# Optimization experiments

Hardware: AMD Instinct MI355X
Metric: run time of the kernel (lower is better)

The kernel has to match this reference:

```python
import jax, jax.numpy as jnp
import numpy as np

N_HEADS = 12


def setup_inputs() -> dict:
    key = jax.random.key(0)
    ks = jax.random.split(key, 3)
    B, N, C = 32, 1024, 768
    x = jax.random.normal(ks[0], (B, N, C), dtype=jnp.float32)
    w_qkv = jax.random.normal(ks[1], (C, 3 * C), dtype=jnp.float32) * (1.0 / np.sqrt(C))
    b_qkv = jnp.zeros((3 * C,), dtype=jnp.float32)
    w_out = jax.random.normal(ks[2], (C, C), dtype=jnp.float32) * (1.0 / np.sqrt(C))
    b_out = jnp.zeros((C,), dtype=jnp.float32)
    return {"x": x, "w_qkv": w_qkv, "b_qkv": b_qkv, "w_out": w_out, "b_out": b_out}


def reference(x, w_qkv, b_qkv, w_out, b_out):
    B, N, C = x.shape
    H = N_HEADS
    D = C // H  # head_dim
    qkv = (x @ w_qkv + b_qkv).reshape(B, N, 3, H, D)
    qkv = jnp.transpose(qkv, (2, 0, 3, 1, 4))
    q, k, v = qkv[0], qkv[1], qkv[2]
    # channel attention: k^T @ v -> (B,H,D,D), scaled by sqrt(head_dim)
    attn = jnp.einsum("bhnd,bhne->bhde", k, v) / np.sqrt(D).astype(np.float32)
    attn = jax.nn.softmax(attn, axis=-1)
    # attn @ q^T -> (B,H,D,N); swapaxes -> (B,H,N,D)
    out = jnp.einsum("bhde,bhne->bhnd", attn, q)
    # ProjOut: merge heads (B,N,C) + Dense(C)
    out = jnp.transpose(out, (0, 2, 1, 3)).reshape(B, N, C)
    return out @ w_out + b_out
```

## Files before the change

kernel.cpp:

```cpp
#include <hip/hip_runtime.h>
#include <hip/hip_bf16.h>
#include <stdint.h>
#include <stddef.h>

#define B_ 32
#define N_ 1024
#define C_ 768
#define H_ 12
#define D_ 64
#define M_ (B_*N_)
#define TC_ (3*C_)

typedef __bf16 bf16_t;
typedef __attribute__((ext_vector_type(8))) __bf16 bf16x8;
typedef __attribute__((ext_vector_type(4))) __bf16 bf16x4;
typedef __attribute__((ext_vector_type(4))) float  f32x4;

#define MFMA16(a,b,c) __builtin_amdgcn_mfma_f32_16x16x32_bf16(a,b,c,0,0,0)

__device__ __forceinline__ void lds_load16(const void* g, void* l) {
  __builtin_amdgcn_global_load_lds(
      (const __attribute__((address_space(1))) void*)g,
      (__attribute__((address_space(3))) void*)l, 16, 0, 0);
}

__global__ void cvt_bf16(const float* __restrict__ in, bf16_t* __restrict__ out, int n) {
  int i = (blockIdx.x * 256 + threadIdx.x) * 8;
  if (i >= n) return;
  const float4 a = *(const float4*)(in + i);
  const float4 b = *(const float4*)(in + i + 4);
  bf16x8 r;
  r[0]=(bf16_t)a.x; r[1]=(bf16_t)a.y; r[2]=(bf16_t)a.z; r[3]=(bf16_t)a.w;
  r[4]=(bf16_t)b.x; r[5]=(bf16_t)b.y; r[6]=(bf16_t)b.z; r[7]=(bf16_t)b.w;
  *(bf16x8*)(out + i) = r;
}

__global__ void transpose_cvt(const float* __restrict__ in, bf16_t* __restrict__ out,
                              int R, int Cc) {
  __shared__ float t[32][33];
  const int c0 = blockIdx.x * 32, r0 = blockIdx.y * 32;
  const int tx = threadIdx.x & 31, ty = threadIdx.x >> 5;
  #pragma unroll
  for (int k = 0; k < 4; ++k)
    t[ty + k*8][tx] = in[(size_t)(r0 + ty + k*8)*Cc + c0 + tx];
  __syncthreads();
  #pragma unroll
  for (int k = 0; k < 4; ++k)
    out[(size_t)(c0 + ty + k*8)*R + r0 + tx] = (bf16_t)t[tx][ty + k*8];
}

template<int MODE>
__global__ __launch_bounds__(256, 2)
void gemm_bt(const bf16_t* __restrict__ A, const bf16_t* __restrict__ BT,
             const float* __restrict__ bias, float* __restrict__ Cout,
             bf16_t* __restrict__ qh,
             bf16_t* __restrict__ kthi, bf16_t* __restrict__ vthi,
             int K, int Ndim, int nbx)
{
  __shared__ __align__(16) char smem[34816];
  bf16_t* As   = (bf16_t*)smem;
  bf16_t* Bs   = (bf16_t*)(smem + 8192);
  bf16_t* tile = (bf16_t*)smem;

  const int nwg = gridDim.x;
  const int cpx = nwg >> 3;
  const int bid = blockIdx.x;
  const int swz = (bid & 7) * cpx + (bid >> 3);
  const int bx  = swz % nbx;
  const int by  = swz / nbx;

  const int tid  = threadIdx.x;
  const int wave = tid >> 6;
  const int lane = tid & 63;
  const int rowBase = by * 128;
  const int colBase = bx * 128;
  const int wr = (wave >> 1) * 64;
  const int wc = (wave &  1) * 64;
  const int fr = lane & 15;
  const int fo = (lane >> 4) * 8;
  const int e  = tid * 8;
  const int r0t = e >> 5;
  const int c0t = e & 31;

  const bf16_t* Ap = A  + (size_t)(rowBase + r0t) * K + c0t;
  const bf16_t* Bp = BT + (size_t)(colBase + r0t) * K + c0t;

  f32x4 acc[4][4] = {{0.f,0.f,0.f,0.f}};

  for (int k0 = 0; k0 < K; k0 += 32) {
    lds_load16(Ap + k0,                 &As[wave*512]);
    lds_load16(Ap + (size_t)64*K + k0,  &As[2048 + wave*512]);
    lds_load16(Bp + k0,                 &Bs[wave*512]);
    lds_load16(Bp + (size_t)64*K + k0,  &Bs[2048 + wave*512]);
    __syncthreads();
    bf16x8 af[4], bfv[4];
    #pragma unroll
    for (int m = 0; m < 4; ++m) af[m]  = *(const bf16x8*)&As[(wr + m*16 + fr)*32 + fo];
    #pragma unroll
    for (int n = 0; n < 4; ++n) bfv[n] = *(const bf16x8*)&Bs[(wc + n*16 + fr)*32 + fo];
    #pragma unroll
    for (int m = 0; m < 4; ++m)
      #pragma unroll
      for (int n = 0; n < 4; ++n)
        acc[m][n] = MFMA16(af[m], bfv[n], acc[m][n]);
    __syncthreads();
  }

  if (MODE == 0) {
    #pragma unroll
    for (int n = 0; n < 4; ++n) {
      const int gc = colBase + wc + n*16 + fr;
      const float bb = bias[gc];
      #pragma unroll
      for (int m = 0; m < 4; ++m) {
        const int gr = rowBase + wr + m*16 + ((lane >> 4) << 2);
        #pragma unroll
        for (int j = 0; j < 4; ++j)
          Cout[(size_t)(gr + j)*Ndim + gc] = acc[m][n][j] + bb;
      }
    }
  } else {
    #pragma unroll
    for (int n = 0; n < 4; ++n) {
      const int c  = wc + n*16 + fr;
      const float bb = bias[colBase + c];
      #pragma unroll
      for (int m = 0; m < 4; ++m) {
        const int r0 = wr + m*16 + ((lane >> 4) << 2);
        bf16x4 hv;
        hv[0]=(bf16_t)(acc[m][n][0]+bb); hv[1]=(bf16_t)(acc[m][n][1]+bb);
        hv[2]=(bf16_t)(acc[m][n][2]+bb); hv[3]=(bf16_t)(acc[m][n][3]+bb);
        *(bf16x4*)&tile[c*136 + r0] = hv;
      }
    }
    __syncthreads();
    const int s   = colBase / C_;
    const int b   = rowBase >> 10;
    const int nn0 = rowBase & (N_ - 1);
    if (s == 0) {
      const int r  = tid >> 1, ch = tid & 1;
      const int h  = (colBase >> 6) + ch;
      bf16_t* dst = qh + (((size_t)b*H_ + h)*N_ + nn0 + r)*D_;
      #pragma unroll
      for (int i0 = 0; i0 < 64; i0 += 8) {
        bf16x8 vv;
        #pragma unroll
        for (int i = 0; i < 8; ++i) vv[i] = tile[(ch*64 + i0 + i)*136 + r];
        *(bf16x8*)&dst[i0] = vv;
      }
    } else {
      const int c  = tid >> 1, rh = tid & 1;
      const int rem = colBase + c - s*C_;
      const int h = rem >> 6, d = rem & 63;
      bf16_t* dst = (s == 1 ? kthi : vthi)
                    + (((size_t)b*H_ + h)*D_ + d)*N_ + nn0 + rh*64;
      #pragma unroll
      for (int i0 = 0; i0 < 64; i0 += 8)
        *(bf16x8*)&dst[i0] = *(const bf16x8*)&tile[c*136 + rh*64 + i0];
    }
  }
}

__global__ __launch_bounds__(256, 2)
void attn_softmax_k(const bf16_t* __restrict__ kthi, const bf16_t* __restrict__ vthi,
                    bf16_t* __restrict__ attn)
{
  __shared__ float tile[64][65];
  const int bh = blockIdx.x;
  const int tid = threadIdx.x, wave = tid >> 6, lane = tid & 63;
  const int fr = lane & 15, fo = (lane >> 4) * 8;
  const size_t base = (size_t)bh * D_ * N_;
  f32x4 acc[4][4] = {{0.f,0.f,0.f,0.f}};
  const int k0lo = wave * 256;
  #pragma unroll 1
  for (int k0 = k0lo; k0 < k0lo + 256; k0 += 32) {
    bf16x8 ah[4], bhv[4];
    #pragma unroll
    for (int m = 0; m < 4; ++m)
      ah[m] = *(const bf16x8*)&kthi[base + (size_t)(m*16 + fr)*N_ + k0 + fo];
    #pragma unroll
    for (int n = 0; n < 4; ++n)
      bhv[n] = *(const bf16x8*)&vthi[base + (size_t)(n*16 + fr)*N_ + k0 + fo];
    #pragma unroll
    for (int m = 0; m < 4; ++m)
      #pragma unroll
      for (int n = 0; n < 4; ++n)
        acc[m][n] = MFMA16(ah[m], bhv[n], acc[m][n]);
  }
  for (int w = 0; w < 4; ++w) {
    if (wave == w) {
      #pragma unroll
      for (int m = 0; m < 4; ++m)
        #pragma unroll
        for (int n = 0; n < 4; ++n) {
          const int row = m*16 + ((lane >> 4) << 2);
          const int col = n*16 + fr;
          #pragma unroll
          for (int j = 0; j < 4; ++j) {
            if (w == 0) tile[row+j][col]  = acc[m][n][j];
            else        tile[row+j][col] += acc[m][n][j];
          }
        }
    }
    __syncthreads();
  }
  if (tid < 64) {
    float mx = -3.0e38f;
    #pragma unroll
    for (int c = 0; c < 64; ++c) mx = fmaxf(mx, tile[tid][c]);
    mx *= 0.125f;
    float ssum = 0.f;
    #pragma unroll
    for (int c = 0; c < 64; ++c) {
      const float ev = __expf(tile[tid][c]*0.125f - mx);
      tile[tid][c] = ev;
      ssum += ev;
    }
    const float inv = 1.0f / ssum;
    bf16_t* ao = attn + (size_t)bh * D_ * D_ + tid * D_;
    #pragma unroll
    for (int c = 0; c < 64; ++c) ao[c] = (bf16_t)(tile[tid][c] * inv);
  }
}

__global__ __launch_bounds__(256, 2)
void attn_apply(const bf16_t* __restrict__ qh, const bf16_t* __restrict__ attn,
                bf16_t* __restrict__ y2)
{
  const int bh = blockIdx.y;
  const int b = bh / H_, h = bh - b*H_;
  const int tid = threadIdx.x, wave = tid >> 6, lane = tid & 63;
  const int fr = lane & 15, fo = (lane >> 4) * 8;
  const int n0 = blockIdx.x * 256 + wave * 64;
  const bf16_t* qb = qh   + (size_t)bh * N_ * D_;
  const bf16_t* ab = attn + (size_t)bh * D_ * D_;
  f32x4 acc[4][4] = {{0.f,0.f,0.f,0.f}};
  #pragma unroll
  for (int k0 = 0; k0 < 64; k0 += 32) {
    bf16x8 af[4], bfv[4];
    #pragma unroll
    for (int m = 0; m < 4; ++m)
      af[m] = *(const bf16x8*)&qb[(size_t)(n0 + m*16 + fr)*D_ + k0 + fo];
    #pragma unroll
    for (int n = 0; n < 4; ++n)
      bfv[n] = *(const bf16x8*)&ab[(n*16 + fr)*D_ + k0 + fo];
    #pragma unroll
    for (int m = 0; m < 4; ++m)
      #pragma unroll
      for (int n = 0; n < 4; ++n)
        acc[m][n] = MFMA16(af[m], bfv[n], acc[m][n]);
  }
  #pragma unroll
  for (int m = 0; m < 4; ++m) {
    const int nr = n0 + m*16 + ((lane >> 4) << 2);
    #pragma unroll
    for (int n = 0; n < 4; ++n) {
      const int d = n*16 + fr;
      #pragma unroll
      for (int j = 0; j < 4; ++j)
        y2[(size_t)(b*N_ + nr + j)*C_ + h*D_ + d] = (bf16_t)acc[m][n][j];
    }
  }
}

extern "C" void kernel_launch(void* const* d_in, const int* in_sizes, int n_in,
                              void* d_out, int out_size, void* d_ws, size_t ws_size,
                              hipStream_t stream)
{
  (void)in_sizes; (void)n_in; (void)out_size;
  const float* x     = (const float*)d_in[0];
  const float* w_qkv = (const float*)d_in[1];
  const float* b_qkv = (const float*)d_in[2];
  const float* w_out = (const float*)d_in[3];
  const float* b_out = (const float*)d_in[4];
  float* out = (float*)d_out;

  const size_t sz_xb   = (size_t)M_*C_*2;
  const size_t sz_wq   = (size_t)TC_*C_*2;
  const size_t sz_wo   = (size_t)C_*C_*2;
  const size_t sz_qh   = (size_t)B_*H_*N_*D_*2;
  const size_t sz_kv   = (size_t)B_*H_*D_*N_*2;
  const size_t sz_attn = (size_t)B_*H_*D_*D_*2;

  char* p = (char*)d_ws;
  bf16_t* xb    = (bf16_t*)p; p += sz_xb;
  bf16_t* wqkvT = (bf16_t*)p; p += sz_wq;
  bf16_t* woutT = (bf16_t*)p; p += sz_wo;
  bf16_t* qh    = (bf16_t*)p; p += sz_qh;
  bf16_t* kthi  = (bf16_t*)p; p += sz_kv;
  bf16_t* vthi  = (bf16_t*)p; p += sz_kv;
  bf16_t* attn  = (bf16_t*)p; p += sz_attn;
  const size_t base_need = (size_t)(p - (char*)d_ws);
  bf16_t* y2 = xb;

  if (ws_size < base_need) return;

  cvt_bf16<<<dim3((M_*C_)/2048), 256, 0, stream>>>(x, xb, M_*C_);
  transpose_cvt<<<dim3(TC_/32, C_/32), 256, 0, stream>>>(w_qkv, wqkvT, C_, TC_);
  transpose_cvt<<<dim3(C_/32,  C_/32), 256, 0, stream>>>(w_out, woutT, C_, C_);

  gemm_bt<1><<<dim3((TC_/128)*(M_/128)), 256, 0, stream>>>(
      xb, wqkvT, b_qkv, nullptr, qh, kthi, vthi, C_, 0, TC_/128);

  attn_softmax_k<<<dim3(B_*H_), 256, 0, stream>>>(kthi, vthi, attn);

  attn_apply<<<dim3(N_/256, B_*H_), 256, 0, stream>>>(qh, attn, y2);

  gemm_bt<0><<<dim3((C_/128)*(M_/128)), 256, 0, stream>>>(
      y2, woutT, b_out, out, nullptr, nullptr, nullptr, C_, C_, C_/128);
}
```

Measured before the change: 300.9 us.

## Fold attention into per-batch output weights and switch GEMM to 32x32 MFMA

Removes the attn_apply pass and its y2 intermediate by composing each batch's attention matrices with the output projection weights into a per-batch weight matrix. The final GEMM then reads q directly in head-major layout. The GEMM core moves from 16x16x32 to 32x32x16 MFMA and adds an XOR swizzle on the LDS layout to reduce bank conflicts. This trades a large activation round trip for a small per-batch weight composition, at the cost of an extra bf16 rounding of the composed weights.

```diff
diff --git a/kernel.cpp b/kernel.cpp
--- a/kernel.cpp
+++ b/kernel.cpp
@@ -15,8 +15,10 @@
 typedef __attribute__((ext_vector_type(8))) __bf16 bf16x8;
 typedef __attribute__((ext_vector_type(4))) __bf16 bf16x4;
 typedef __attribute__((ext_vector_type(4))) float  f32x4;
+typedef __attribute__((ext_vector_type(16))) float f32x16;
 
 #define MFMA16(a,b,c) __builtin_amdgcn_mfma_f32_16x16x32_bf16(a,b,c,0,0,0)
+#define MFMA32(a,b,c) __builtin_amdgcn_mfma_f32_32x32x16_bf16(a,b,c,0,0,0)
 
 __device__ __forceinline__ void lds_load16(const void* g, void* l) {
   __builtin_amdgcn_global_load_lds(
@@ -55,7 +57,7 @@
              const float* __restrict__ bias, float* __restrict__ Cout,
              bf16_t* __restrict__ qh,
              bf16_t* __restrict__ kthi, bf16_t* __restrict__ vthi,
-             int K, int Ndim, int nbx)
+             int K, int nbx, size_t bt_bstride)
 {
   __shared__ __align__(16) char smem[34816];
   bf16_t* As   = (bf16_t*)smem;
@@ -76,62 +78,91 @@
   const int colBase = bx * 128;
   const int wr = (wave >> 1) * 64;
   const int wc = (wave &  1) * 64;
-  const int fr = lane & 15;
-  const int fo = (lane >> 4) * 8;
-  const int e  = tid * 8;
-  const int r0t = e >> 5;
-  const int c0t = e & 31;
-
-  const bf16_t* Ap = A  + (size_t)(rowBase + r0t) * K + c0t;
-  const bf16_t* Bp = BT + (size_t)(colBase + r0t) * K + c0t;
-
-  f32x4 acc[4][4] = {{0.f,0.f,0.f,0.f}};
+  const int l31 = lane & 31;
+  const int lhi = lane >> 5;
+  const int xr  = (lane >> 1) & 3;
+  const int r0t = tid >> 2;
+  const int c0s = (((tid & 3) ^ ((tid >> 3) & 3)) << 3);
+
+  const bf16_t* Bp = BT + (MODE == 3 ? (size_t)(rowBase >> 10) * bt_bstride : 0)
+                        + (size_t)(colBase + r0t) * K + c0s;
+  const bf16_t* Ap;
+  if (MODE == 3) {
+    const int gr = rowBase + r0t;
+    Ap = A + (size_t)(gr >> 10) * (H_ * N_ * D_) + (size_t)(gr & (N_ - 1)) * D_ + c0s;
+  } else {
+    Ap = A + (size_t)(rowBase + r0t) * K + c0s;
+  }
+
+  f32x16 acc[2][2];
+  #pragma unroll
+  for (int m = 0; m < 2; ++m)
+    #pragma unroll
+    for (int n = 0; n < 2; ++n)
+      #pragma unroll
+      for (int j = 0; j < 16; ++j) acc[m][n][j] = 0.f;
 
   for (int k0 = 0; k0 < K; k0 += 32) {
-    lds_load16(Ap + k0,                 &As[wave*512]);
-    lds_load16(Ap + (size_t)64*K + k0,  &As[2048 + wave*512]);
-    lds_load16(Bp + k0,                 &Bs[wave*512]);
-    lds_load16(Bp + (size_t)64*K + k0,  &Bs[2048 + wave*512]);
+    const bf16_t* a0;
+    size_t a_half;
+    if (MODE == 3) { a0 = Ap + (size_t)(k0 >> 6) * (N_ * D_) + (k0 & 63); a_half = (size_t)64 * D_; }
+    else           { a0 = Ap + k0;                                        a_half = (size_t)64 * K;  }
+    lds_load16(a0,              &As[wave * 512]);
+    lds_load16(a0 + a_half,     &As[2048 + wave * 512]);
+    lds_load16(Bp + k0,                  &Bs[wave * 512]);
+    lds_load16(Bp + (size_t)64 * K + k0, &Bs[2048 + wave * 512]);
     __syncthreads();
-    bf16x8 af[4], bfv[4];
-    #pragma unroll
-    for (int m = 0; m < 4; ++m) af[m]  = *(const bf16x8*)&As[(wr + m*16 + fr)*32 + fo];
-    #pragma unroll
-    for (int n = 0; n < 4; ++n) bfv[n] = *(const bf16x8*)&Bs[(wc + n*16 + fr)*32 + fo];
-    #pragma unroll
-    for (int m = 0; m < 4; ++m)
-      #pragma unroll
-      for (int n = 0; n < 4; ++n)
-        acc[m][n] = MFMA16(af[m], bfv[n], acc[m][n]);
+    bf16x8 af[2][2], bfv[2][2];
+    #pragma unroll
+    for (int m = 0; m < 2; ++m)
+      #pragma unroll
+      for (int kk = 0; kk < 2; ++kk)
+        af[m][kk] = *(const bf16x8*)&As[(wr + m*32 + l31)*32 + (((2*kk + lhi) ^ xr) << 3)];
+    #pragma unroll
+    for (int n = 0; n < 2; ++n)
+      #pragma unroll
+      for (int kk = 0; kk < 2; ++kk)
+        bfv[n][kk] = *(const bf16x8*)&Bs[(wc + n*32 + l31)*32 + (((2*kk + lhi) ^ xr) << 3)];
+    #pragma unroll
+    for (int m = 0; m < 2; ++m)
+      #pragma unroll
+      for (int n = 0; n < 2; ++n)
+        #pragma unroll
+        for (int kk = 0; kk < 2; ++kk)
+          acc[m][n] = MFMA32(af[m][kk], bfv[n][kk], acc[m][n]);
     __syncthreads();
   }
 
-  if (MODE == 0) {
-    #pragma unroll
-    for (int n = 0; n < 4; ++n) {
-      const int gc = colBase + wc + n*16 + fr;
+  if (MODE == 3) {
+    #pragma unroll
+    for (int n = 0; n < 2; ++n) {
+      const int gc = colBase + wc + n*32 + l31;
       const float bb = bias[gc];
       #pragma unroll
-      for (int m = 0; m < 4; ++m) {
-        const int gr = rowBase + wr + m*16 + ((lane >> 4) << 2);
-        #pragma unroll
-        for (int j = 0; j < 4; ++j)
-          Cout[(size_t)(gr + j)*Ndim + gc] = acc[m][n][j] + bb;
-      }
+      for (int m = 0; m < 2; ++m)
+        #pragma unroll
+        for (int g = 0; g < 4; ++g) {
+          const int gr = rowBase + wr + m*32 + g*8 + lhi*4;
+          #pragma unroll
+          for (int j = 0; j < 4; ++j)
+            Cout[(size_t)(gr + j)*C_ + gc] = acc[m][n][4*g + j] + bb;
+        }
     }
   } else {
     #pragma unroll
-    for (int n = 0; n < 4; ++n) {
-      const int c  = wc + n*16 + fr;
+    for (int n = 0; n < 2; ++n) {
+      const int c  = wc + n*32 + l31;
       const float bb = bias[colBase + c];
       #pragma unroll
-      for (int m = 0; m < 4; ++m) {
-        const int r0 = wr + m*16 + ((lane >> 4) << 2);
-        bf16x4 hv;
-        hv[0]=(bf16_t)(acc[m][n][0]+bb); hv[1]=(bf16_t)(acc[m][n][1]+bb);
-        hv[2]=(bf16_t)(acc[m][n][2]+bb); hv[3]=(bf16_t)(acc[m][n][3]+bb);
-        *(bf16x4*)&tile[c*136 + r0] = hv;
-      }
+      for (int m = 0; m < 2; ++m)
+        #pragma unroll
+        for (int g = 0; g < 4; ++g) {
+          const int r0 = wr + m*32 + g*8 + lhi*4;
+          bf16x4 hv;
+          hv[0]=(bf16_t)(acc[m][n][4*g+0]+bb); hv[1]=(bf16_t)(acc[m][n][4*g+1]+bb);
+          hv[2]=(bf16_t)(acc[m][n][4*g+2]+bb); hv[3]=(bf16_t)(acc[m][n][4*g+3]+bb);
+          *(bf16x4*)&tile[c*136 + r0] = hv;
+        }
     }
     __syncthreads();
     const int s   = colBase / C_;
@@ -163,9 +194,10 @@
 
 __global__ __launch_bounds__(256, 2)
 void attn_softmax_k(const bf16_t* __restrict__ kthi, const bf16_t* __restrict__ vthi,
-                    bf16_t* __restrict__ attn)
+                    bf16_t* __restrict__ attnT)
 {
   __shared__ float tile[64][65];
+  __shared__ float invs[64];
   const int bh = blockIdx.x;
   const int tid = threadIdx.x, wave = tid >> 6, lane = tid & 63;
   const int fr = lane & 15, fo = (lane >> 4) * 8;
@@ -216,49 +248,57 @@
       tile[tid][c] = ev;
       ssum += ev;
     }
-    const float inv = 1.0f / ssum;
-    bf16_t* ao = attn + (size_t)bh * D_ * D_ + tid * D_;
-    #pragma unroll
-    for (int c = 0; c < 64; ++c) ao[c] = (bf16_t)(tile[tid][c] * inv);
+    invs[tid] = 1.0f / ssum;
+  }
+  __syncthreads();
+  if (tid < 64) {
+    bf16_t* ao = attnT + (size_t)bh * D_ * D_ + tid * D_;
+    #pragma unroll
+    for (int d0 = 0; d0 < 64; d0 += 8) {
+      bf16x8 vv;
+      #pragma unroll
+      for (int i = 0; i < 8; ++i) vv[i] = (bf16_t)(tile[d0+i][tid] * invs[d0+i]);
+      *(bf16x8*)&ao[d0] = vv;
+    }
   }
 }
 
 __global__ __launch_bounds__(256, 2)
-void attn_apply(const bf16_t* __restrict__ qh, const bf16_t* __restrict__ attn,
-                bf16_t* __restrict__ y2)
+void compose_w2(const bf16_t* __restrict__ woutT, const bf16_t* __restrict__ attnT,
+                bf16_t* __restrict__ w2t)
 {
+  const int jb = blockIdx.x;
   const int bh = blockIdx.y;
   const int b = bh / H_, h = bh - b*H_;
   const int tid = threadIdx.x, wave = tid >> 6, lane = tid & 63;
   const int fr = lane & 15, fo = (lane >> 4) * 8;
-  const int n0 = blockIdx.x * 256 + wave * 64;
-  const bf16_t* qb = qh   + (size_t)bh * N_ * D_;
-  const bf16_t* ab = attn + (size_t)bh * D_ * D_;
-  f32x4 acc[4][4] = {{0.f,0.f,0.f,0.f}};
-  #pragma unroll
-  for (int k0 = 0; k0 < 64; k0 += 32) {
-    bf16x8 af[4], bfv[4];
-    #pragma unroll
-    for (int m = 0; m < 4; ++m)
-      af[m] = *(const bf16x8*)&qb[(size_t)(n0 + m*16 + fr)*D_ + k0 + fo];
+  const bf16_t* at = attnT + (size_t)bh * D_ * D_;
+  f32x4 acc[2][4] = {{0.f,0.f,0.f,0.f}};
+  #pragma unroll
+  for (int kk = 0; kk < 2; ++kk) {
+    bf16x8 af[2], bfv[4];
+    #pragma unroll
+    for (int m = 0; m < 2; ++m)
+      af[m] = *(const bf16x8*)&woutT[(size_t)(jb*128 + wave*32 + m*16 + fr)*C_ + h*64 + kk*32 + fo];
     #pragma unroll
     for (int n = 0; n < 4; ++n)
-      bfv[n] = *(const bf16x8*)&ab[(n*16 + fr)*D_ + k0 + fo];
-    #pragma unroll
-    for (int m = 0; m < 4; ++m)
+      bfv[n] = *(const bf16x8*)&at[(n*16 + fr)*64 + kk*32 + fo];
+    #pragma unroll
+    for (int m = 0; m < 2; ++m)
       #pragma unroll
       for (int n = 0; n < 4; ++n)
         acc[m][n] = MFMA16(af[m], bfv[n], acc[m][n]);
   }
-  #pragma unroll
-  for (int m = 0; m < 4; ++m) {
-    const int nr = n0 + m*16 + ((lane >> 4) << 2);
+  bf16_t* wb = w2t + (size_t)b * C_ * C_;
+  #pragma unroll
+  for (int m = 0; m < 2; ++m) {
+    const int j = jb*128 + wave*32 + m*16 + ((lane >> 4) << 2);
     #pragma unroll
     for (int n = 0; n < 4; ++n) {
-      const int d = n*16 + fr;
-      #pragma unroll
-      for (int j = 0; j < 4; ++j)
-        y2[(size_t)(b*N_ + nr + j)*C_ + h*D_ + d] = (bf16_t)acc[m][n][j];
+      const int e = n*16 + fr;
+      #pragma unroll
+      for (int jj = 0; jj < 4; ++jj)
+        wb[(size_t)(j + jj)*C_ + h*64 + e] = (bf16_t)acc[m][n][jj];
     }
   }
 }
@@ -289,9 +329,9 @@
   bf16_t* qh    = (bf16_t*)p; p += sz_qh;
   bf16_t* kthi  = (bf16_t*)p; p += sz_kv;
   bf16_t* vthi  = (bf16_t*)p; p += sz_kv;
-  bf16_t* attn  = (bf16_t*)p; p += sz_attn;
+  bf16_t* attnT = (bf16_t*)p; p += sz_attn;
   const size_t base_need = (size_t)(p - (char*)d_ws);
-  bf16_t* y2 = xb;
+  bf16_t* w2t = xb;
 
   if (ws_size < base_need) return;
 
@@ -300,12 +340,12 @@
   transpose_cvt<<<dim3(C_/32,  C_/32), 256, 0, stream>>>(w_out, woutT, C_, C_);
 
   gemm_bt<1><<<dim3((TC_/128)*(M_/128)), 256, 0, stream>>>(
-      xb, wqkvT, b_qkv, nullptr, qh, kthi, vthi, C_, 0, TC_/128);
-
-  attn_softmax_k<<<dim3(B_*H_), 256, 0, stream>>>(kthi, vthi, attn);
-
-  attn_apply<<<dim3(N_/256, B_*H_), 256, 0, stream>>>(qh, attn, y2);
-
-  gemm_bt<0><<<dim3((C_/128)*(M_/128)), 256, 0, stream>>>(
-      y2, woutT, b_out, out, nullptr, nullptr, nullptr, C_, C_, C_/128);
-}
+      xb, wqkvT, b_qkv, nullptr, qh, kthi, vthi, C_, TC_/128, 0);
+
+  attn_softmax_k<<<dim3(B_*H_), 256, 0, stream>>>(kthi, vthi, attnT);
+
+  compose_w2<<<dim3(C_/128, B_*H_), 256, 0, stream>>>(woutT, attnT, w2t);
+
+  gemm_bt<3><<<dim3((C_/128)*(M_/128)), 256, 0, stream>>>(
+      qh, w2t, b_out, out, nullptr, nullptr, nullptr, C_, C_/128, (size_t)C_*C_);
+}
```

Result: slower. 314.6 us (+4.6%).
